# Kernel tuning notes

Measured on AMD Instinct MI355X. Metric: run time of the kernel, lower is better.

The kernel has to match this reference:

```python
import jax, jax.numpy as jnp
import numpy as np
import math

D_MODEL = 1024
N_HEADS = 16
D_K = D_MODEL // N_HEADS  # 64


def setup_inputs() -> dict:
    key = jax.random.key(0)
    ks = jax.random.split(key, 12)
    B, S = 2, 2048
    scale = 1.0 / math.sqrt(D_MODEL)
    inp = {
        'q': jax.random.normal(ks[0], (B, S, D_MODEL), jnp.float32),
        'k': jax.random.normal(ks[1], (B, S, D_MODEL), jnp.float32),
        'v': jax.random.normal(ks[2], (B, S, D_MODEL), jnp.float32),
        'Wq': jax.random.normal(ks[3], (D_MODEL, D_MODEL), jnp.float32) * scale,
        'bq': jnp.zeros((D_MODEL,), jnp.float32),
        'Wk': jax.random.normal(ks[4], (D_MODEL, D_MODEL), jnp.float32) * scale,
        'bk': jnp.zeros((D_MODEL,), jnp.float32),
        'Wv': jax.random.normal(ks[5], (D_MODEL, D_MODEL), jnp.float32) * scale,
        'bv': jnp.zeros((D_MODEL,), jnp.float32),
        'Wo': jax.random.normal(ks[6], (D_MODEL, D_MODEL), jnp.float32) * scale,
        'bo': jnp.zeros((D_MODEL,), jnp.float32),
        'phase': jax.random.normal(ks[7], (N_HEADS, 1, 1), jnp.float32),
    }
    return inp


def _split_heads(x, B):
    # (B, S, D) -> (B, H, S, d_k)
    return x.reshape(B, -1, N_HEADS, D_K).transpose(0, 2, 1, 3)


def _phase_sync(x, phase):
    # x: (B, H, S, d_k); treat [first half, second half] as complex pair,
    # rotate by per-head phase: (re + i*im) * exp(i*phase)
    half = D_K // 2
    xr, xi = x[..., :half], x[..., half:]
    c = jnp.cos(phase)[None]  # (1, H, 1, 1)
    s = jnp.sin(phase)[None]
    return jnp.concatenate([xr * c - xi * s, xr * s + xi * c], axis=-1)


def reference(q, k, v, Wq, bq, Wk, bk, Wv, bv, Wo, bo, phase):
    B = q.shape[0]
    qh = _split_heads(q @ Wq.T + bq, B)
    kh = _split_heads(k @ Wk.T + bk, B)
    vh = _split_heads(v @ Wv.T + bv, B)
    qh = _phase_sync(qh, phase)
    kh = _phase_sync(kh, phase)
    scores = jnp.einsum('bhqd,bhkd->bhqk', qh, kh) / math.sqrt(D_K)
    attn = jax.nn.softmax(scores, axis=-1)  # dropout is identity in eval
    out = jnp.einsum('bhqk,bhkd->bhqd', attn, vh)
    out = out.transpose(0, 2, 1, 3).reshape(B, -1, D_MODEL)
    return out @ Wo.T + bo
```

## Files before the change

### kernel.cpp

```cpp
#include <hip/hip_runtime.h>
#include <hip/hip_bf16.h>


typedef short bf16x8 __attribute__((ext_vector_type(8)));
typedef float f32x4 __attribute__((ext_vector_type(4)));
typedef unsigned short u16;
typedef unsigned short u16x8 __attribute__((ext_vector_type(8)));
typedef unsigned short u16x4 __attribute__((ext_vector_type(4)));

static __device__ __forceinline__ u16 f2bf(float x) {
    __hip_bfloat16 b = __float2bfloat16(x);
    return *reinterpret_cast<u16*>(&b);
}
static __device__ __forceinline__ bf16x8 g8(const u16* p) {
    return *reinterpret_cast<const bf16x8*>(p);
}
static __device__ __forceinline__ float fast_exp2(float x) {
#if __has_builtin(__builtin_amdgcn_exp2f)
    return __builtin_amdgcn_exp2f(x);
#else
    return exp2f(x);
#endif
}
static __device__ __forceinline__ u16x8 cvt8(const float4& a, const float4& b) {
    u16x8 r;
    r[0] = f2bf(a.x); r[1] = f2bf(a.y); r[2] = f2bf(a.z); r[3] = f2bf(a.w);
    r[4] = f2bf(b.x); r[5] = f2bf(b.y); r[6] = f2bf(b.z); r[7] = f2bf(b.w);
    return r;
}

#define SWZ(row, col) ((row) * 32 + ((col) ^ ((((row) >> 1) & 3) << 3)))

__global__ void k_splitW(const float* __restrict__ w0, const float* __restrict__ w1,
                         const float* __restrict__ w2, const float* __restrict__ w3,
                         u16* __restrict__ h0, u16* __restrict__ h1,
                         u16* __restrict__ h2, u16* __restrict__ h3) {
    const int i = blockIdx.x * 256 + threadIdx.x;
    const float* s;
    u16* H;
    if (blockIdx.y == 0) { s = w0; H = h0; }
    else if (blockIdx.y == 1) { s = w1; H = h1; }
    else if (blockIdx.y == 2) { s = w2; H = h2; }
    else { s = w3; H = h3; }
    float4 val = reinterpret_cast<const float4*>(s)[i];
    u16x4 h;
    h[0] = f2bf(val.x); h[1] = f2bf(val.y);
    h[2] = f2bf(val.z); h[3] = f2bf(val.w);
    reinterpret_cast<u16x4*>(H)[i] = h;
}

__global__ __launch_bounds__(256) void k_gemm(
    const float* __restrict__ qf, const float* __restrict__ kf,
    const float* __restrict__ vf,
    const u16* __restrict__ Wqh, const u16* __restrict__ Wkh,
    const u16* __restrict__ Wvh,
    const float* __restrict__ bq, const float* __restrict__ bk,
    const float* __restrict__ bv_,
    const float* __restrict__ phase,
    u16* __restrict__ Qrh, u16* __restrict__ Krh,
    u16* __restrict__ VTh) {
    __shared__ __attribute__((aligned(16))) u16 sA[128 * 32];
    __shared__ __attribute__((aligned(16))) u16 sB[128 * 32];

    const int z = blockIdx.z;
    const float* Af;
    const u16* Bh;
    const float* bias;
    if (z == 0) { Af = qf; Bh = Wqh; bias = bq; }
    else if (z == 1) { Af = kf; Bh = Wkh; bias = bk; }
    else { Af = vf; Bh = Wvh; bias = bv_; }

    const int flat = blockIdx.y * 8 + blockIdx.x;
    const int tau = (flat & 7) * 32 + (flat >> 3);
    const int bx = tau & 7, by = tau >> 3;

    const int t = threadIdx.x;
    const int l = t & 63, w = t >> 6;
    const int wr = w >> 1, wc = w & 1;
    const int m0 = by * 128, n0 = bx * 128;

    const int srow = t >> 2;
    const int scol = (t & 3) * 8;
    const float* pA0 = Af + (size_t)(m0 + srow) * 1024 + scol;
    const float* pA1 = Af + (size_t)(m0 + 64 + srow) * 1024 + scol;
    const u16* pB0 = Bh + (size_t)(n0 + srow) * 1024 + scol;
    const u16* pB1 = Bh + (size_t)(n0 + 64 + srow) * 1024 + scol;
    const int so0 = SWZ(srow, scol);
    const int so1 = SWZ(srow + 64, scol);

    u16x8 rA0, rA1;
    bf16x8 rB0, rB1;
    auto load_tiles = [&](int kk) {
        const int ko = kk * 32;
        float4 a00 = *reinterpret_cast<const float4*>(pA0 + ko);
        float4 a01 = *reinterpret_cast<const float4*>(pA0 + ko + 4);
        float4 a10 = *reinterpret_cast<const float4*>(pA1 + ko);
        float4 a11 = *reinterpret_cast<const float4*>(pA1 + ko + 4);
        rB0 = g8(pB0 + ko);
        rB1 = g8(pB1 + ko);
        rA0 = cvt8(a00, a01);
        rA1 = cvt8(a10, a11);
    };

    f32x4 acc[4][4];
#pragma unroll
    for (int m = 0; m < 4; ++m)
#pragma unroll
        for (int n = 0; n < 4; ++n) acc[m][n] = (f32x4){0.f, 0.f, 0.f, 0.f};

    const int fr = l & 15;
    const int fk = (l >> 4) * 8;
    const int ar = wr * 64 + fr;
    const int br = wc * 64 + fr;

    load_tiles(0);
    for (int kk = 0; kk < 32; ++kk) {
        __syncthreads();
        *reinterpret_cast<u16x8*>(&sA[so0]) = rA0;
        *reinterpret_cast<u16x8*>(&sA[so1]) = rA1;
        *reinterpret_cast<bf16x8*>(&sB[so0]) = rB0;
        *reinterpret_cast<bf16x8*>(&sB[so1]) = rB1;
        __syncthreads();
        if (kk < 31) load_tiles(kk + 1);

        bf16x8 fa[4], fb[4];
#pragma unroll
        for (int m = 0; m < 4; ++m)
            fa[m] = *reinterpret_cast<const bf16x8*>(&sA[SWZ(ar + m * 16, fk)]);
#pragma unroll
        for (int n = 0; n < 4; ++n)
            fb[n] = *reinterpret_cast<const bf16x8*>(&sB[SWZ(br + n * 16, fk)]);
#pragma unroll
        for (int m = 0; m < 4; ++m)
#pragma unroll
            for (int n = 0; n < 4; ++n)
                acc[m][n] = __builtin_amdgcn_mfma_f32_16x16x32_bf16(fa[m], fb[n], acc[m][n], 0, 0, 0);
    }

    const int er4 = (l >> 4) * 4;
    float bvv[4];
#pragma unroll
    for (int n = 0; n < 4; ++n) bvv[n] = bias[n0 + wc * 64 + n * 16 + fr];

    if (z == 2) {
#pragma unroll
        for (int m = 0; m < 4; ++m) {
            const int row0 = m0 + wr * 64 + m * 16 + er4;
            const int bb = row0 >> 11;
            const int ss = row0 & 2047;
#pragma unroll
            for (int n = 0; n < 4; ++n) {
                const int col = n0 + wc * 64 + n * 16 + fr;
                const int hh_ = col >> 6, dd = col & 63;
                u16x4 vv;
#pragma unroll
                for (int r = 0; r < 4; ++r) vv[r] = f2bf(acc[m][n][r] + bvv[n]);
                *reinterpret_cast<u16x4*>(
                    &VTh[((size_t)(bb * 16 + hh_) * 64 + dd) * 2048 + ss]) = vv;
            }
        }
    } else {
        u16* Dh = z ? Krh : Qrh;
        const float sc = z ? 1.0f : 0.18033688011112042f;
        const int head = bx * 2 + wc;
        float sv, cv;
        sincosf(phase[head], &sv, &cv);
#pragma unroll
        for (int m = 0; m < 4; ++m)
#pragma unroll
            for (int n = 0; n < 2; ++n) {
#pragma unroll
                for (int r = 0; r < 4; ++r) {
                    const float xr = acc[m][n][r] + bvv[n];
                    const float xi = acc[m][n + 2][r] + bvv[n + 2];
                    const float o0 = (xr * cv - xi * sv) * sc;
                    const float o1 = (xr * sv + xi * cv) * sc;
                    const int row = m0 + wr * 64 + m * 16 + er4 + r;
                    const size_t i0 = (size_t)row * 1024 + head * 64 + n * 16 + fr;
                    Dh[i0] = f2bf(o0);
                    Dh[i0 + 32] = f2bf(o1);
                }
            }
    }
}

__global__ __launch_bounds__(256) void k_gemm1(
    const u16* __restrict__ Ah, const u16* __restrict__ Bh,
    const float* __restrict__ bias, float* __restrict__ C) {
    __shared__ __attribute__((aligned(16))) u16 sA[128 * 32];
    __shared__ __attribute__((aligned(16))) u16 sB[128 * 32];

    const int flat = blockIdx.y * 8 + blockIdx.x;
    const int tau = (flat & 7) * 32 + (flat >> 3);
    const int bx = tau & 7, by = tau >> 3;

    const int t = threadIdx.x;
    const int l = t & 63, w = t >> 6;
    const int wr = w >> 1, wc = w & 1;
    const int m0 = by * 128, n0 = bx * 128;

    const int srow = t >> 2;
    const int scol = (t & 3) * 8;
    const u16* pA0 = Ah + (size_t)(m0 + srow) * 1024 + scol;
    const u16* pA1 = Ah + (size_t)(m0 + 64 + srow) * 1024 + scol;
    const u16* pB0 = Bh + (size_t)(n0 + srow) * 1024 + scol;
    const u16* pB1 = Bh + (size_t)(n0 + 64 + srow) * 1024 + scol;
    const int so0 = SWZ(srow, scol);
    const int so1 = SWZ(srow + 64, scol);

    bf16x8 rA0, rA1, rB0, rB1;
    auto load_tiles = [&](int kk) {
        const int ko = kk * 32;
        rA0 = g8(pA0 + ko); rA1 = g8(pA1 + ko);
        rB0 = g8(pB0 + ko); rB1 = g8(pB1 + ko);
    };

    f32x4 acc[4][4];
#pragma unroll
    for (int m = 0; m < 4; ++m)
#pragma unroll
        for (int n = 0; n < 4; ++n) acc[m][n] = (f32x4){0.f, 0.f, 0.f, 0.f};

    const int fr = l & 15;
    const int fk = (l >> 4) * 8;
    const int ar = wr * 64 + fr;
    const int br = wc * 64 + fr;

    load_tiles(0);
    for (int kk = 0; kk < 32; ++kk) {
        __syncthreads();
        *reinterpret_cast<bf16x8*>(&sA[so0]) = rA0;
        *reinterpret_cast<bf16x8*>(&sA[so1]) = rA1;
        *reinterpret_cast<bf16x8*>(&sB[so0]) = rB0;
        *reinterpret_cast<bf16x8*>(&sB[so1]) = rB1;
        __syncthreads();
        if (kk < 31) load_tiles(kk + 1);

        bf16x8 fa[4], fb[4];
#pragma unroll
        for (int m = 0; m < 4; ++m)
            fa[m] = *reinterpret_cast<const bf16x8*>(&sA[SWZ(ar + m * 16, fk)]);
#pragma unroll
        for (int n = 0; n < 4; ++n)
            fb[n] = *reinterpret_cast<const bf16x8*>(&sB[SWZ(br + n * 16, fk)]);
#pragma unroll
        for (int m = 0; m < 4; ++m)
#pragma unroll
            for (int n = 0; n < 4; ++n)
                acc[m][n] = __builtin_amdgcn_mfma_f32_16x16x32_bf16(fa[m], fb[n], acc[m][n], 0, 0, 0);
    }

    const int er4 = (l >> 4) * 4;
    float bvv[4];
#pragma unroll
    for (int n = 0; n < 4; ++n) bvv[n] = bias[n0 + wc * 64 + n * 16 + fr];
#pragma unroll
    for (int m = 0; m < 4; ++m)
#pragma unroll
        for (int n = 0; n < 4; ++n) {
            const int col = n0 + wc * 64 + n * 16 + fr;
            const size_t rb = (size_t)(m0 + wr * 64 + m * 16 + er4) * 1024 + col;
#pragma unroll
            for (int r = 0; r < 4; ++r) C[rb + (size_t)r * 1024] = acc[m][n][r] + bvv[n];
        }
}

#define SM_M2 17.312340490667562f

#define ATTN_TILE(SK, SV)                                                      \
  {                                                                            \
    f32x4 s[2][4];                                                             \
    _Pragma("unroll") for (int qm = 0; qm < 2; ++qm)                           \
      _Pragma("unroll") for (int n = 0; n < 4; ++n)                            \
        s[qm][n] = (f32x4){-SM_M2, -SM_M2, -SM_M2, -SM_M2};                    \
    _Pragma("unroll") for (int n = 0; n < 4; ++n)                              \
      _Pragma("unroll") for (int ks = 0; ks < 2; ++ks) {                       \
        bf16x8 bkh = *reinterpret_cast<const bf16x8*>(                         \
            &SK[(n * 16 + fr) * 64 + ((ks * 32 + fk) ^ rswz)]);                \
        _Pragma("unroll") for (int qm = 0; qm < 2; ++qm)                       \
          s[qm][n] = __builtin_amdgcn_mfma_f32_16x16x32_bf16(aqh[qm][ks], bkh, s[qm][n], 0, 0, 0); \
      }                                                                        \
    _Pragma("unroll") for (int qm = 0; qm < 2; ++qm)                           \
      _Pragma("unroll") for (int n = 0; n < 4; ++n)                            \
        _Pragma("unroll") for (int r = 0; r < 4; ++r) {                        \
          const float p = fast_exp2(s[qm][n][r]);                              \
          const int prow = w * 32 + qm * 16 + (l >> 4) * 4 + r;                \
          const int pcol = (n * 16 + (l & 15)) ^ ((prow & 7) << 3);            \
          sPh[prow * 64 + pcol] = f2bf(p);                                     \
        }                                                                      \
    bf16x8 bph[2][2];                                                          \
    _Pragma("unroll") for (int qm = 0; qm < 2; ++qm)                           \
      _Pragma("unroll") for (int ks = 0; ks < 2; ++ks)                         \
        bph[qm][ks] = *reinterpret_cast<const bf16x8*>(                        \
            &sPh[(w * 32 + qm * 16 + fr) * 64 + ((ks * 32 + fk) ^ rswz)]);     \
    _Pragma("unroll") for (int m = 0; m < 4; ++m)                              \
      _Pragma("unroll") for (int ks = 0; ks < 2; ++ks) {                       \
        bf16x8 avh = *reinterpret_cast<const bf16x8*>(                         \
            &SV[(m * 16 + fr) * 64 + ((ks * 32 + fk) ^ rswz)]);                \
        _Pragma("unroll") for (int qm = 0; qm < 2; ++qm)                       \
          aco[qm][m] = __builtin_amdgcn_mfma_f32_16x16x32_bf16(avh, bph[qm][ks], aco[qm][m], 0, 0, 0); \
      }                                                                        \
    _Pragma("unroll") for (int qm = 0; qm < 2; ++qm)                           \
      _Pragma("unroll") for (int ks = 0; ks < 2; ++ks)                         \
        acl[qm] = __builtin_amdgcn_mfma_f32_16x16x32_bf16(vone, bph[qm][ks], acl[qm], 0, 0, 0); \
  }

#define ATTN_STAGE(SK, SV)                                                     \
  {                                                                            \
    _Pragma("unroll") for (int i = 0; i < 2; ++i) {                            \
      *reinterpret_cast<bf16x8*>(&SK[soff[i]]) = rKh[i];                       \
      *reinterpret_cast<bf16x8*>(&SV[soff[i]]) = rVh[i];                       \
    }                                                                          \
  }

__global__ __launch_bounds__(256) void k_attn(
    const u16* __restrict__ Qh,
    const u16* __restrict__ Kh,
    const u16* __restrict__ VTh,
    u16* __restrict__ AOh) {
    __shared__ __attribute__((aligned(16))) u16 sK0[4096];
    __shared__ __attribute__((aligned(16))) u16 sK1[4096];
    __shared__ __attribute__((aligned(16))) u16 sV0[4096];
    __shared__ __attribute__((aligned(16))) u16 sV1[4096];
    __shared__ __attribute__((aligned(16))) u16 sPh[128 * 64];

    const int t = threadIdx.x;
    const int l = t & 63, w = t >> 6;
    const int flat = blockIdx.y * 16 + blockIdx.x;
    const int tau = (flat & 7) * 64 + (flat >> 3);
    const int q0 = (tau & 15) * 128;
    const int bh = tau >> 4;
    const int b = bh >> 4, h = bh & 15;
    const size_t qrow0 = (size_t)b * 2048 + q0;

    const u16* Qb_h = Qh + qrow0 * 1024 + h * 64;
    const u16* Kb_h = Kh + (size_t)b * 2048 * 1024 + h * 64;
    const u16* Vb_h = VTh + (size_t)bh * 64 * 2048;

    const int fr = l & 15;
    const int fk = (l >> 4) * 8;

    bf16x8 aqh[2][2];
#pragma unroll
    for (int qm = 0; qm < 2; ++qm)
#pragma unroll
        for (int ks = 0; ks < 2; ++ks) {
            const size_t qo = (size_t)(w * 32 + qm * 16 + fr) * 1024 + ks * 32 + fk;
            aqh[qm][ks] = g8(Qb_h + qo);
        }

    bf16x8 vone;
#pragma unroll
    for (int j = 0; j < 8; ++j) vone[j] = (short)0x3F80;

    f32x4 aco[2][4];
    f32x4 acl[2];
#pragma unroll
    for (int qm = 0; qm < 2; ++qm) {
        acl[qm] = (f32x4){0.f, 0.f, 0.f, 0.f};
#pragma unroll
        for (int m = 0; m < 4; ++m) aco[qm][m] = (f32x4){0.f, 0.f, 0.f, 0.f};
    }

    const int sr = t >> 3, sc = (t & 7) * 8;
    bf16x8 rKh[2], rVh[2];
    auto load_kv = [&](int tt) {
        const int kv0 = tt * 64;
#pragma unroll
        for (int i = 0; i < 2; ++i) {
            const int r2 = sr + i * 32;
            rKh[i] = g8(Kb_h + (size_t)(kv0 + r2) * 1024 + sc);
            rVh[i] = g8(Vb_h + (size_t)r2 * 2048 + kv0 + sc);
        }
    };
    int soff[2];
#pragma unroll
    for (int i = 0; i < 2; ++i) {
        const int r2 = sr + i * 32;
        soff[i] = r2 * 64 + (sc ^ ((r2 & 7) << 3));
    }
    const int rswz = (fr & 7) << 3;

    load_kv(0);
    ATTN_STAGE(sK0, sV0);
    __syncthreads();

    for (int tt = 0; tt < 32; tt += 2) {
        load_kv(tt + 1);
        ATTN_TILE(sK0, sV0);
        ATTN_STAGE(sK1, sV1);
        __syncthreads();
        if (tt + 2 < 32) load_kv(tt + 2);
        ATTN_TILE(sK1, sV1);
        if (tt + 2 < 32) ATTN_STAGE(sK0, sV0);
        __syncthreads();
    }

#pragma unroll
    for (int qm = 0; qm < 2; ++qm) {
        const float inv = 1.0f / acl[qm][0];
#pragma unroll
        for (int m = 0; m < 4; ++m) aco[qm][m] *= inv;
    }

    float* Ol = reinterpret_cast<float*>(
        (w == 0) ? sK0 : (w == 1) ? sK1 : (w == 2) ? sV0 : sV1);
#pragma unroll
    for (int qm = 0; qm < 2; ++qm) {
        const int qr = qm * 16 + (l & 15);
        const int sw = (qr & 7) << 3;
#pragma unroll
        for (int m = 0; m < 4; ++m)
#pragma unroll
            for (int r = 0; r < 4; ++r)
                Ol[qr * 64 + ((m * 16 + (l >> 4) * 4 + r) ^ sw)] = aco[qm][m][r];
    }
#pragma unroll
    for (int it = 0; it < 4; ++it) {
        const int qr = (l >> 3) + it * 8;
        const int cb = (l & 7) * 8;
        const int sw = (qr & 7) << 3;
        const float* srcp = &Ol[qr * 64 + (cb ^ sw)];
        u16x8 oh;
#pragma unroll
        for (int j = 0; j < 8; ++j) oh[j] = f2bf(srcp[j]);
        const size_t ob = (qrow0 + w * 32 + qr) * 1024 + h * 64 + cb;
        *reinterpret_cast<u16x8*>(&AOh[ob]) = oh;
    }
}

extern "C" void kernel_launch(void* const* d_in, const int* in_sizes, int n_in,
                              void* d_out, int out_size, void* d_ws, size_t ws_size,
                              hipStream_t stream) {
    const float* q = (const float*)d_in[0];
    const float* k = (const float*)d_in[1];
    const float* v = (const float*)d_in[2];
    const float* Wq = (const float*)d_in[3];
    const float* bq = (const float*)d_in[4];
    const float* Wk = (const float*)d_in[5];
    const float* bk = (const float*)d_in[6];
    const float* Wv = (const float*)d_in[7];
    const float* bv = (const float*)d_in[8];
    const float* Wo = (const float*)d_in[9];
    const float* bo = (const float*)d_in[10];
    const float* phase = (const float*)d_in[11];
    float* out = (float*)d_out;

    char* ws = (char*)d_ws;
    const size_t MB = 1u << 20;
    u16* Wq_h = (u16*)(ws + 0 * MB);
    u16* Wk_h = (u16*)(ws + 2 * MB);
    u16* Wv_h = (u16*)(ws + 4 * MB);
    u16* Wo_h = (u16*)(ws + 6 * MB);
    u16* QR_h = (u16*)(ws + 64 * MB);
    u16* KR_h = (u16*)(ws + 80 * MB);
    u16* VT_h = (u16*)(ws + 96 * MB);
    u16* AO_h = (u16*)(ws + 16 * MB);

    k_splitW<<<dim3(1024, 4), 256, 0, stream>>>(Wq, Wk, Wv, Wo,
                                                Wq_h, Wk_h, Wv_h, Wo_h);
    k_gemm<<<dim3(8, 32, 3), 256, 0, stream>>>(
        q, k, v, Wq_h, Wk_h, Wv_h,
        bq, bk, bv, phase, QR_h, KR_h, VT_h);
    k_attn<<<dim3(16, 32), 256, 0, stream>>>(QR_h, KR_h, VT_h, AO_h);
    k_gemm1<<<dim3(8, 32), 256, 0, stream>>>(AO_h, Wo_h, bo, out);
    (void)in_sizes; (void)n_in; (void)out_size; (void)ws_size;
}
```

Baseline: 128.1 us.

## Double-buffer GEMM LDS tiles and stage bf16 operands via global_load_lds

New measurement: 124.4 us. 2.9% less time.

```diff
diff --git a/kernel.cpp b/kernel.cpp
--- a/kernel.cpp
+++ b/kernel.cpp
@@ -21,6 +21,11 @@
 #else
     return exp2f(x);
 #endif
+}
+static __device__ __forceinline__ void gl16(const u16* g, u16* l) {
+    __builtin_amdgcn_global_load_lds(
+        (const __attribute__((address_space(1))) void*)g,
+        (__attribute__((address_space(3))) void*)l, 16, 0, 0);
 }
 static __device__ __forceinline__ u16x8 cvt8(const float4& a, const float4& b) {
     u16x8 r;
@@ -59,8 +64,10 @@
     const float* __restrict__ phase,
     u16* __restrict__ Qrh, u16* __restrict__ Krh,
     u16* __restrict__ VTh) {
-    __shared__ __attribute__((aligned(16))) u16 sA[128 * 32];
-    __shared__ __attribute__((aligned(16))) u16 sB[128 * 32];
+    __shared__ __attribute__((aligned(16))) u16 sA0[128 * 32];
+    __shared__ __attribute__((aligned(16))) u16 sA1[128 * 32];
+    __shared__ __attribute__((aligned(16))) u16 sB0[128 * 32];
+    __shared__ __attribute__((aligned(16))) u16 sB1[128 * 32];
 
     const int z = blockIdx.z;
     const float* Af;
@@ -78,28 +85,40 @@
     const int l = t & 63, w = t >> 6;
     const int wr = w >> 1, wc = w & 1;
     const int m0 = by * 128, n0 = bx * 128;
+    const int fr = l & 15;
+    const int fk = (l >> 4) * 8;
+    const int ar = wr * 64 + fr;
+    const int br = wc * 64 + fr;
+
+    const int grow = w * 32 + (l >> 2);
+    const int colx = ((l & 3) * 8) ^ (((grow >> 1) & 3) << 3);
+    const int lb0 = (w * 2) * 512, lb1 = (w * 2 + 1) * 512;
+    const u16* pB0 = Bh + (size_t)(n0 + grow) * 1024 + colx;
+    const u16* pB1 = Bh + (size_t)(n0 + grow + 16) * 1024 + colx;
 
     const int srow = t >> 2;
     const int scol = (t & 3) * 8;
     const float* pA0 = Af + (size_t)(m0 + srow) * 1024 + scol;
     const float* pA1 = Af + (size_t)(m0 + 64 + srow) * 1024 + scol;
-    const u16* pB0 = Bh + (size_t)(n0 + srow) * 1024 + scol;
-    const u16* pB1 = Bh + (size_t)(n0 + 64 + srow) * 1024 + scol;
     const int so0 = SWZ(srow, scol);
     const int so1 = SWZ(srow + 64, scol);
 
-    u16x8 rA0, rA1;
-    bf16x8 rB0, rB1;
-    auto load_tiles = [&](int kk) {
+    float4 a00, a01, a10, a11;
+    auto loadA = [&](int kk) {
         const int ko = kk * 32;
-        float4 a00 = *reinterpret_cast<const float4*>(pA0 + ko);
-        float4 a01 = *reinterpret_cast<const float4*>(pA0 + ko + 4);
-        float4 a10 = *reinterpret_cast<const float4*>(pA1 + ko);
-        float4 a11 = *reinterpret_cast<const float4*>(pA1 + ko + 4);
-        rB0 = g8(pB0 + ko);
-        rB1 = g8(pB1 + ko);
-        rA0 = cvt8(a00, a01);
-        rA1 = cvt8(a10, a11);
+        a00 = *reinterpret_cast<const float4*>(pA0 + ko);
+        a01 = *reinterpret_cast<const float4*>(pA0 + ko + 4);
+        a10 = *reinterpret_cast<const float4*>(pA1 + ko);
+        a11 = *reinterpret_cast<const float4*>(pA1 + ko + 4);
+    };
+    auto stageB = [&](u16* SB, int kk) {
+        const int ko = kk * 32;
+        gl16(pB0 + ko, &SB[lb0]);
+        gl16(pB1 + ko, &SB[lb1]);
+    };
+    auto writeA = [&](u16* SA) {
+        *reinterpret_cast<u16x8*>(&SA[so0]) = cvt8(a00, a01);
+        *reinterpret_cast<u16x8*>(&SA[so1]) = cvt8(a10, a11);
     };
 
     f32x4 acc[4][4];
@@ -108,33 +127,40 @@
 #pragma unroll
         for (int n = 0; n < 4; ++n) acc[m][n] = (f32x4){0.f, 0.f, 0.f, 0.f};
 
-    const int fr = l & 15;
-    const int fk = (l >> 4) * 8;
-    const int ar = wr * 64 + fr;
-    const int br = wc * 64 + fr;
-
-    load_tiles(0);
-    for (int kk = 0; kk < 32; ++kk) {
-        __syncthreads();
-        *reinterpret_cast<u16x8*>(&sA[so0]) = rA0;
-        *reinterpret_cast<u16x8*>(&sA[so1]) = rA1;
-        *reinterpret_cast<bf16x8*>(&sB[so0]) = rB0;
-        *reinterpret_cast<bf16x8*>(&sB[so1]) = rB1;
-        __syncthreads();
-        if (kk < 31) load_tiles(kk + 1);
-
+    auto compute = [&](const u16* SA, const u16* SB) {
         bf16x8 fa[4], fb[4];
 #pragma unroll
         for (int m = 0; m < 4; ++m)
-            fa[m] = *reinterpret_cast<const bf16x8*>(&sA[SWZ(ar + m * 16, fk)]);
+            fa[m] = *reinterpret_cast<const bf16x8*>(&SA[SWZ(ar + m * 16, fk)]);
 #pragma unroll
         for (int n = 0; n < 4; ++n)
-            fb[n] = *reinterpret_cast<const bf16x8*>(&sB[SWZ(br + n * 16, fk)]);
+            fb[n] = *reinterpret_cast<const bf16x8*>(&SB[SWZ(br + n * 16, fk)]);
 #pragma unroll
         for (int m = 0; m < 4; ++m)
 #pragma unroll
             for (int n = 0; n < 4; ++n)
                 acc[m][n] = __builtin_amdgcn_mfma_f32_16x16x32_bf16(fa[m], fb[n], acc[m][n], 0, 0, 0);
+    };
+
+    loadA(0);
+    stageB(sB0, 0);
+    writeA(sA0);
+    __syncthreads();
+
+    for (int kk = 0; kk < 32; kk += 2) {
+        loadA(kk + 1);
+        stageB(sB1, kk + 1);
+        compute(sA0, sB0);
+        writeA(sA1);
+        __syncthreads();
+        const bool more = (kk + 2 < 32);
+        if (more) {
+            loadA(kk + 2);
+            stageB(sB0, kk + 2);
+        }
+        compute(sA1, sB1);
+        if (more) writeA(sA0);
+        __syncthreads();
     }
 
     const int er4 = (l >> 4) * 4;
@@ -187,8 +213,10 @@
 __global__ __launch_bounds__(256) void k_gemm1(
     const u16* __restrict__ Ah, const u16* __restrict__ Bh,
     const float* __restrict__ bias, float* __restrict__ C) {
-    __shared__ __attribute__((aligned(16))) u16 sA[128 * 32];
-    __shared__ __attribute__((aligned(16))) u16 sB[128 * 32];
+    __shared__ __attribute__((aligned(16))) u16 sA0[128 * 32];
+    __shared__ __attribute__((aligned(16))) u16 sA1[128 * 32];
+    __shared__ __attribute__((aligned(16))) u16 sB0[128 * 32];
+    __shared__ __attribute__((aligned(16))) u16 sB1[128 * 32];
 
     const int flat = blockIdx.y * 8 + blockIdx.x;
     const int tau = (flat & 7) * 32 + (flat >> 3);
@@ -198,56 +226,57 @@
     const int l = t & 63, w = t >> 6;
     const int wr = w >> 1, wc = w & 1;
     const int m0 = by * 128, n0 = bx * 128;
-
-    const int srow = t >> 2;
-    const int scol = (t & 3) * 8;
-    const u16* pA0 = Ah + (size_t)(m0 + srow) * 1024 + scol;
-    const u16* pA1 = Ah + (size_t)(m0 + 64 + srow) * 1024 + scol;
-    const u16* pB0 = Bh + (size_t)(n0 + srow) * 1024 + scol;
-    const u16* pB1 = Bh + (size_t)(n0 + 64 + srow) * 1024 + scol;
-    const int so0 = SWZ(srow, scol);
-    const int so1 = SWZ(srow + 64, scol);
-
-    bf16x8 rA0, rA1, rB0, rB1;
-    auto load_tiles = [&](int kk) {
-        const int ko = kk * 32;
-        rA0 = g8(pA0 + ko); rA1 = g8(pA1 + ko);
-        rB0 = g8(pB0 + ko); rB1 = g8(pB1 + ko);
-    };
-
-    f32x4 acc[4][4];
-#pragma unroll
-    for (int m = 0; m < 4; ++m)
-#pragma unroll
-        for (int n = 0; n < 4; ++n) acc[m][n] = (f32x4){0.f, 0.f, 0.f, 0.f};
-
     const int fr = l & 15;
     const int fk = (l >> 4) * 8;
     const int ar = wr * 64 + fr;
     const int br = wc * 64 + fr;
 
-    load_tiles(0);
-    for (int kk = 0; kk < 32; ++kk) {
-        __syncthreads();
-        *reinterpret_cast<bf16x8*>(&sA[so0]) = rA0;
-        *reinterpret_cast<bf16x8*>(&sA[so1]) = rA1;
-        *reinterpret_cast<bf16x8*>(&sB[so0]) = rB0;
-        *reinterpret_cast<bf16x8*>(&sB[so1]) = rB1;
-        __syncthreads();
-        if (kk < 31) load_tiles(kk + 1);
-
+    const int grow = w * 32 + (l >> 2);
+    const int colx = ((l & 3) * 8) ^ (((grow >> 1) & 3) << 3);
+    const int lb0 = (w * 2) * 512, lb1 = (w * 2 + 1) * 512;
+    const u16* pA0 = Ah + (size_t)(m0 + grow) * 1024 + colx;
+    const u16* pA1 = Ah + (size_t)(m0 + grow + 16) * 1024 + colx;
+    const u16* pB0 = Bh + (size_t)(n0 + grow) * 1024 + colx;
+    const u16* pB1 = Bh + (size_t)(n0 + grow + 16) * 1024 + colx;
+
+    auto stage = [&](u16* SA, u16* SB, int kk) {
+        const int ko = kk * 32;
+        gl16(pA0 + ko, &SA[lb0]);
+        gl16(pA1 + ko, &SA[lb1]);
+        gl16(pB0 + ko, &SB[lb0]);
+        gl16(pB1 + ko, &SB[lb1]);
+    };
+
+    f32x4 acc[4][4];
+#pragma unroll
+    for (int m = 0; m < 4; ++m)
+#pragma unroll
+        for (int n = 0; n < 4; ++n) acc[m][n] = (f32x4){0.f, 0.f, 0.f, 0.f};
+
+    auto compute = [&](const u16* SA, const u16* SB) {
         bf16x8 fa[4], fb[4];
 #pragma unroll
         for (int m = 0; m < 4; ++m)
-            fa[m] = *reinterpret_cast<const bf16x8*>(&sA[SWZ(ar + m * 16, fk)]);
+            fa[m] = *reinterpret_cast<const bf16x8*>(&SA[SWZ(ar + m * 16, fk)]);
 #pragma unroll
         for (int n = 0; n < 4; ++n)
-            fb[n] = *reinterpret_cast<const bf16x8*>(&sB[SWZ(br + n * 16, fk)]);
+            fb[n] = *reinterpret_cast<const bf16x8*>(&SB[SWZ(br + n * 16, fk)]);
 #pragma unroll
         for (int m = 0; m < 4; ++m)
 #pragma unroll
             for (int n = 0; n < 4; ++n)
                 acc[m][n] = __builtin_amdgcn_mfma_f32_16x16x32_bf16(fa[m], fb[n], acc[m][n], 0, 0, 0);
+    };
+
+    stage(sA0, sB0, 0);
+    __syncthreads();
+    for (int kk = 0; kk < 32; kk += 2) {
+        stage(sA1, sB1, kk + 1);
+        compute(sA0, sB0);
+        __syncthreads();
+        if (kk + 2 < 32) stage(sA0, sB0, kk + 2);
+        compute(sA1, sB1);
+        __syncthreads();
     }
 
     const int er4 = (l >> 4) * 4;
```
